# Kernel tuning notes

Hardware: AMD Instinct MI355X
Metric: run time of the kernel (lower is better)

The kernel has to match this reference:

```python
import jax, jax.numpy as jnp
import numpy as np

NUM_ITEMS = 1000000   # catalog size; id == NUM_ITEMS is the padding item
B, S = 512, 200       # batch, sequence length
M, SUB = 8, 32        # pq_m bytes per item, sub-embedding size (embedding_size = M*SUB = 256)
NUM_CENTROIDS = 256   # uint8 code range


def setup_inputs() -> dict:
    key = jax.random.key(0)
    k1, k2, k3 = jax.random.split(key, 3)
    input_ids = jax.random.randint(k1, (B, S), 0, NUM_ITEMS + 1, dtype=jnp.int64)
    # item_codes: PQ code table, one byte (0..255) per item per code-byte
    item_codes = jax.random.randint(k2, (NUM_ITEMS + 1, M), 0, NUM_CENTROIDS, dtype=jnp.int32)
    # centroids: per-byte codebooks, uniform init as in tf.random_uniform_initializer()
    centroids = jax.random.uniform(k3, (M, NUM_CENTROIDS, SUB), dtype=jnp.float32)
    return {"input_ids": input_ids, "item_codes": item_codes, "centroids": centroids}


def reference(input_ids, item_codes, centroids):
    # codes[b,s,i] = PQ byte i of item input_ids[b,s]
    codes = item_codes[input_ids]                                  # [B, S, M] int32
    byte_idx = jnp.arange(codes.shape[-1])[None, None, :]          # [1, 1, M]
    # gather centroid vector per (byte, code): centroids[i, codes[b,s,i], :]
    sub_emb = centroids[byte_idx, codes]                           # [B, S, M, SUB]
    b, s = input_ids.shape
    return sub_emb.reshape(b, s, codes.shape[-1] * centroids.shape[-1])  # [B, S, M*SUB]
```

## Files before the change

### kernel.cpp

```cpp
#include <hip/hip_runtime.h>
#include <hip/hip_bf16.h>


typedef float f4  __attribute__((ext_vector_type(4)));
typedef int   v4i __attribute__((ext_vector_type(4)));

#define M_BYTES 8
#define SUB_DIM 32
#define EMB     (M_BYTES * SUB_DIM)
#define TOK_PER_BLOCK 128
#define BLOCK 256

__global__ __launch_bounds__(BLOCK) void ItemCodeLayer_30253749633338_kernel(
    const int*   __restrict__ ids,
    const int*   __restrict__ codes,
    const float* __restrict__ cent,
    float*       __restrict__ out,
    int n_tokens)
{
    __shared__ int s_codes[TOK_PER_BLOCK * M_BYTES];

    const int tid  = threadIdx.x;
    const int base = blockIdx.x * TOK_PER_BLOCK;

    {
        const int tA = tid >> 1;
        const int h  = tid & 1;
        int id = (base + tA < n_tokens) ? ids[base + tA] : 0;
        v4i row = __builtin_nontemporal_load(
            reinterpret_cast<const v4i*>(codes + (size_t)id * M_BYTES + h * 4));
        *reinterpret_cast<v4i*>(&s_codes[tA * M_BYTES + h * 4]) = row;
    }
    __syncthreads();

    const int wave = tid >> 6;
    const int l    = tid & 63;
    const int lm   = l >> 3;
    const int lj   = (l & 7) * 4;
    const float* centBase = cent + (size_t)lm * 256 * SUB_DIM + lj;

    #pragma unroll
    for (int it = 0; it < 32; it += 8) {
        int tk[8];
        f4  v[8];
        #pragma unroll
        for (int u = 0; u < 8; ++u) {
            tk[u] = wave * 32 + it + u;
            int code = s_codes[tk[u] * M_BYTES + lm];
            v[u] = *reinterpret_cast<const f4*>(centBase + (size_t)code * SUB_DIM);
        }
        #pragma unroll
        for (int u = 0; u < 8; ++u) {
            int t = base + tk[u];
            if (t < n_tokens) {
                *reinterpret_cast<f4*>(
                    out + ((size_t)t * EMB + lm * SUB_DIM + lj)) = v[u];
            }
        }
    }
}

extern "C" void kernel_launch(void* const* d_in, const int* in_sizes, int n_in,
                              void* d_out, int out_size, void* d_ws, size_t ws_size,
                              hipStream_t stream) {
    const int*   ids   = (const int*)  d_in[0];
    const int*   codes = (const int*)  d_in[1];
    const float* cent  = (const float*)d_in[2];
    float*       out   = (float*)      d_out;

    const int n_tokens = in_sizes[0];
    const int grid = (n_tokens + TOK_PER_BLOCK - 1) / TOK_PER_BLOCK;

    hipLaunchKernelGGL(ItemCodeLayer_30253749633338_kernel,
                       dim3(grid), dim3(BLOCK), 0, stream,
                       ids, codes, cent, out, n_tokens);
}
```

Measured before the change: 128.6 us.

## Drop LDS staging and barrier; each wave loads its own codes directly

Removes the shared-memory code staging and the block-wide barrier. Each wave now handles 8 tokens and reads ids and code bytes straight from global memory per lane. Blocks shrink from 128 to 32 tokens, so the grid is four times larger. The cost is redundant global code loads (8 lanes read the same byte) and more, smaller blocks, in exchange for removing the sync and raising the number of gathers in flight.

```diff
diff --git a/kernel.cpp b/kernel.cpp
--- a/kernel.cpp
+++ b/kernel.cpp
@@ -1,15 +1,15 @@
 #include <hip/hip_runtime.h>
-#include <hip/hip_bf16.h>
 
 
-typedef float f4  __attribute__((ext_vector_type(4)));
-typedef int   v4i __attribute__((ext_vector_type(4)));
+typedef float f4 __attribute__((ext_vector_type(4)));
 
 #define M_BYTES 8
 #define SUB_DIM 32
 #define EMB     (M_BYTES * SUB_DIM)
-#define TOK_PER_BLOCK 128
-#define BLOCK 256
+#define TPW     8
+#define WAVES   4
+#define TOK_PER_BLOCK (TPW * WAVES)
+#define BLOCK   256
 
 __global__ __launch_bounds__(BLOCK) void ItemCodeLayer_30253749633338_kernel(
     const int*   __restrict__ ids,
@@ -18,43 +18,39 @@
     float*       __restrict__ out,
     int n_tokens)
 {
-    __shared__ int s_codes[TOK_PER_BLOCK * M_BYTES];
+    const int tid  = threadIdx.x;
+    const int l    = tid & 63;
+    const int wave = __builtin_amdgcn_readfirstlane(tid >> 6);
+    const int lm   = l >> 3;
+    const int l4   = l * 4;
 
-    const int tid  = threadIdx.x;
-    const int base = blockIdx.x * TOK_PER_BLOCK;
+    const float* centBase = cent + (size_t)lm * 256 * SUB_DIM + (l & 7) * 4;
 
-    {
-        const int tA = tid >> 1;
-        const int h  = tid & 1;
-        int id = (base + tA < n_tokens) ? ids[base + tA] : 0;
-        v4i row = __builtin_nontemporal_load(
-            reinterpret_cast<const v4i*>(codes + (size_t)id * M_BYTES + h * 4));
-        *reinterpret_cast<v4i*>(&s_codes[tA * M_BYTES + h * 4]) = row;
-    }
-    __syncthreads();
+    const int t0 = blockIdx.x * TOK_PER_BLOCK + wave * TPW;
 
-    const int wave = tid >> 6;
-    const int l    = tid & 63;
-    const int lm   = l >> 3;
-    const int lj   = (l & 7) * 4;
-    const float* centBase = cent + (size_t)lm * 256 * SUB_DIM + lj;
-
-    #pragma unroll
-    for (int it = 0; it < 32; it += 8) {
-        int tk[8];
-        f4  v[8];
+    if (t0 + TPW <= n_tokens) {
+        int c[TPW];
         #pragma unroll
-        for (int u = 0; u < 8; ++u) {
-            tk[u] = wave * 32 + it + u;
-            int code = s_codes[tk[u] * M_BYTES + lm];
-            v[u] = *reinterpret_cast<const f4*>(centBase + (size_t)code * SUB_DIM);
+        for (int k = 0; k < TPW; ++k) {
+            int id = ids[t0 + k];
+            c[k] = __builtin_nontemporal_load(codes + (size_t)id * M_BYTES + lm);
         }
+        f4 v[TPW];
         #pragma unroll
-        for (int u = 0; u < 8; ++u) {
-            int t = base + tk[u];
+        for (int k = 0; k < TPW; ++k)
+            v[k] = *reinterpret_cast<const f4*>(centBase + (size_t)c[k] * SUB_DIM);
+        #pragma unroll
+        for (int k = 0; k < TPW; ++k)
+            *reinterpret_cast<f4*>(out + (size_t)(t0 + k) * EMB + l4) = v[k];
+    } else if (t0 < n_tokens) {
+        #pragma unroll
+        for (int k = 0; k < TPW; ++k) {
+            int t = t0 + k;
             if (t < n_tokens) {
-                *reinterpret_cast<f4*>(
-                    out + ((size_t)t * EMB + lm * SUB_DIM + lj)) = v[u];
+                int id  = ids[t];
+                int cd  = codes[(size_t)id * M_BYTES + lm];
+                f4 val  = *reinterpret_cast<const f4*>(centBase + (size_t)cd * SUB_DIM);
+                *reinterpret_cast<f4*>(out + (size_t)t * EMB + l4) = val;
             }
         }
     }
```

Measured after the change: 133.4 us. 1.04x slower.
